# Optimization experiments

Hardware: AMD Instinct MI355X
Metric: run time of the kernel (lower is better)

Reference implementation:

```python
import jax, jax.numpy as jnp
import numpy as np

T, B, I, H = 1024, 64, 512, 512


def setup_inputs() -> dict:
    key = jax.random.key(0)
    ks = jax.random.split(key, 16)
    s = 0.05  # weight init scale
    inp = {
        "x": jax.random.normal(ks[0], (T, B, I), jnp.float32),
        "h0": jax.random.normal(ks[1], (B, H), jnp.float32),
        "c0": jax.random.normal(ks[2], (B, H), jnp.float32),
        "W_ih0f": jax.random.normal(ks[3], (4 * H, I), jnp.float32) * s,
        "W_hh0f": jax.random.normal(ks[4], (4 * H, H), jnp.float32) * s,
        "b0f": jax.random.normal(ks[5], (4 * H,), jnp.float32) * s,
        "W_ih0b": jax.random.normal(ks[6], (4 * H, I), jnp.float32) * s,
        "W_hh0b": jax.random.normal(ks[7], (4 * H, H), jnp.float32) * s,
        "b0b": jax.random.normal(ks[8], (4 * H,), jnp.float32) * s,
        "W_ih1f": jax.random.normal(ks[9], (4 * H, 2 * H), jnp.float32) * s,
        "W_hh1f": jax.random.normal(ks[10], (4 * H, H), jnp.float32) * s,
        "b1f": jax.random.normal(ks[11], (4 * H,), jnp.float32) * s,
        "W_ih1b": jax.random.normal(ks[12], (4 * H, 2 * H), jnp.float32) * s,
        "W_hh1b": jax.random.normal(ks[13], (4 * H, H), jnp.float32) * s,
        "b1b": jax.random.normal(ks[14], (4 * H,), jnp.float32) * s,
    }
    return inp


def _lstm_dir(x, h0, c0, W_ih, W_hh, b, reverse):
    # x: [T, B, in]; precompute input contribution once (big GEMM)
    xg = jnp.einsum('tbi,gi->tbg', x, W_ih) + b  # [T, B, 4H]

    def step(carry, xt):
        h, c = carry
        g = xt + h @ W_hh.T  # [B, 4H]
        i, f, gg, o = jnp.split(g, 4, axis=-1)  # PyTorch LSTMCell gate order
        i = jax.nn.sigmoid(i)
        f = jax.nn.sigmoid(f)
        gg = jnp.tanh(gg)
        o = jax.nn.sigmoid(o)
        c2 = f * c + i * gg
        h2 = o * jnp.tanh(c2)
        return (h2, c2), h2

    (hT, cT), out = jax.lax.scan(step, (h0, c0), xg, reverse=reverse)
    return out, hT, cT  # out[t] aligned with input time t


def reference(x, h0, c0,
              W_ih0f, W_hh0f, b0f, W_ih0b, W_hh0b, b0b,
              W_ih1f, W_hh1f, b1f, W_ih1b, W_hh1b, b1b):
    layers = [
        ((W_ih0f, W_hh0f, b0f), (W_ih0b, W_hh0b, b0b)),
        ((W_ih1f, W_hh1f, b1f), (W_ih1b, W_hh1b, b1b)),
    ]
    inputs = x
    hn, cn = [], []
    for (fw, bw) in layers:
        # NOTE: original reuses the same init_hidden for every layer/direction
        out_f, hf, cf = _lstm_dir(inputs, h0, c0, *fw, reverse=False)
        out_b, hb, cb = _lstm_dir(inputs, h0, c0, *bw, reverse=True)
        hn.append(jnp.concatenate([hf, hb], axis=1))
        cn.append(jnp.concatenate([cf, cb], axis=1))
        inputs = jnp.concatenate([out_f, out_b], axis=2)  # [T, B, 2H]
    hn = jnp.stack(hn, axis=0)  # [L, B, 2H]
    cn = jnp.stack(cn, axis=0)
    return inputs, hn, cn
```

## Files before the change

kernel.cpp:

```cpp
#include <hip/hip_runtime.h>


using bfrag = __attribute__((ext_vector_type(8))) short;
using facc  = __attribute__((ext_vector_type(4))) float;

#define TT 1024
#define NB 64

__device__ __forceinline__ unsigned short f2bf(float f) {
  union { float f; unsigned u; } v; v.f = f;
  unsigned r = v.u + 0x7fffu + ((v.u >> 16) & 1u);
  return (unsigned short)(r >> 16);
}
__device__ __forceinline__ float sigm(float x)  { return 1.f / (1.f + __expf(-x)); }
__device__ __forceinline__ float tanhf_(float x){ return 1.f - 2.f / (__expf(2.f * x) + 1.f); }

__device__ __forceinline__ facc mfma_bf16(bfrag a, bfrag b, facc c) {
  asm("v_mfma_f32_16x16x32_bf16 %0, %1, %2, %0" : "+v"(c) : "v"(a), "v"(b));
  return c;
}

__device__ __forceinline__ bfrag load_h16(const unsigned short* p) {
  union { unsigned long long q[2]; bfrag v; } u;
  const unsigned long long* qp = reinterpret_cast<const unsigned long long*>(p);
  u.q[0] = __hip_atomic_load(qp,     __ATOMIC_RELAXED, __HIP_MEMORY_SCOPE_AGENT);
  u.q[1] = __hip_atomic_load(qp + 1, __ATOMIC_RELAXED, __HIP_MEMORY_SCOPE_AGENT);
  return u.v;
}

__global__ __launch_bounds__(256) void k_cvt_x(const float* __restrict__ x,
                                               unsigned short* __restrict__ xb) {
  int i = blockIdx.x * 256 + threadIdx.x;
  float4 v = reinterpret_cast<const float4*>(x)[i];
  ushort4 o;
  o.x = f2bf(v.x); o.y = f2bf(v.y); o.z = f2bf(v.z); o.w = f2bf(v.w);
  reinterpret_cast<ushort4*>(xb)[i] = o;
}

__global__ __launch_bounds__(256) void k_init(const float* __restrict__ h0,
                                              unsigned short* __restrict__ h0b,
                                              unsigned* __restrict__ flags) {
  int i = blockIdx.x * 256 + threadIdx.x;
  h0b[i] = f2bf(h0[i]);
  if (i < 8192) flags[i] = 0;
}

template <int KX>
__global__ __launch_bounds__(256) void k_pack(const float* __restrict__ Wih,
                                              const float* __restrict__ Whh,
                                              const float* __restrict__ bias,
                                              unsigned short* __restrict__ PW,
                                              float* __restrict__ PB) {
  constexpr int K = KX + 512;
  int tid = blockIdx.x * 256 + threadIdx.x;
  int R = tid / K;
  int k = tid - R * K;
  int g = R >> 4, r = R & 15;
  int q = r >> 2, gate = r & 3;
  int srow = gate * 512 + (g * 4 + q);
  float v = (k < KX) ? Wih[srow * KX + k] : Whh[srow * 512 + (k - KX)];
  int gb = R >> 5, rr = R & 31, cc = k >> 3;
  PW[(size_t)gb * (K / 8) * 272 + cc * 272 + rr * 8 + (k & 7)] = f2bf(v);
  if (k == 0) PB[R] = bias[srow];
}

template <int LAYER>
__global__ __launch_bounds__(512, 2) void k_scan(
    const unsigned short* __restrict__ xin,
    unsigned short* __restrict__ y0,
    float* __restrict__ dout,
    const unsigned short* __restrict__ h0b,
    const float* __restrict__ c0,
    unsigned short* __restrict__ hb,
    const unsigned short* __restrict__ PWf, const unsigned short* __restrict__ PWb,
    const float* __restrict__ PBf, const float* __restrict__ PBb,
    unsigned* __restrict__ flagF, unsigned* __restrict__ flagB) {
  constexpr int KX = (LAYER == 0) ? 512 : 1024;
  constexpr int K  = KX + 512;
  constexpr int CH = K / 8;
  extern __shared__ unsigned short Wlds[];

  const int bid = blockIdx.x;
  const int dir = bid >> 6;
  const int gb  = bid & 63;
  const int tid = threadIdx.x;
  unsigned* flags = dir ? flagB : flagF;
  const unsigned short* pw = (dir ? PWb : PWf) + (size_t)gb * CH * 272;
  const float* pb          = dir ? PBb : PBf;

  for (int i = tid; i < CH * 34; i += 512)
    reinterpret_cast<bfrag*>(Wlds)[i] = reinterpret_cast<const bfrag*>(pw)[i];
  __syncthreads();

  const int w = tid >> 6, lane = tid & 63;
  const int lr = lane & 15, lq = lane >> 4;
  const int grT = w & 1, bT = w >> 1;
  const int b    = bT * 16 + lr;
  const int hcol = (gb * 2 + grT) * 4 + lq;
  const int ldsBase = grT * 128 + lr * 8;
  const float4 bias = *reinterpret_cast<const float4*>(pb + (gb * 2 + grT) * 16 + lq * 4);
  float c = c0[b * 512 + hcol];

  for (int s = 0; s < TT; ++s) {
    const int t = dir ? (TT - 1 - s) : s;

    const unsigned short* xrow = xin + ((size_t)t * NB + b) * KX + lq * 8;
    facc a0 = {0.f, 0.f, 0.f, 0.f}, a1 = {0.f, 0.f, 0.f, 0.f};
    asm volatile("s_nop 3" : "+v"(a0), "+v"(a1));
#pragma unroll 8
    for (int kk = 0; kk < KX / 32; ++kk) {
      bfrag a = *reinterpret_cast<const bfrag*>(Wlds + (size_t)(kk * 4 + lq) * 272 + ldsBase);
      bfrag x = *reinterpret_cast<const bfrag*>(xrow + kk * 32);
      if (kk & 1) a1 = mfma_bf16(a, x, a1); else a0 = mfma_bf16(a, x, a0);
    }

    if (s > 0) {
      if (w == 0) {
        unsigned* fl = flags + lane * 32;
        while (__hip_atomic_load(fl, __ATOMIC_RELAXED, __HIP_MEMORY_SCOPE_AGENT) < (unsigned)s)
          __builtin_amdgcn_s_sleep(1);
      }
      __syncthreads();
    }

    const int tp = dir ? (t + 1) : (t - 1);
    const unsigned short* hrow;
    if (s == 0)               hrow = h0b + (size_t)b * 512 + lq * 8;
    else if constexpr (LAYER == 0)
                              hrow = y0 + ((size_t)tp * NB + b) * 1024 + dir * 512 + lq * 8;
    else                      hrow = hb + (size_t)(((s & 1) ^ 1) * 2 + dir) * 32768 + (size_t)b * 512 + lq * 8;
#pragma unroll 8
    for (int kk = 0; kk < 16; ++kk) {
      bfrag a = *reinterpret_cast<const bfrag*>(Wlds + (size_t)(KX / 8 + kk * 4 + lq) * 272 + ldsBase);
      bfrag h = load_h16(hrow + kk * 32);
      if (kk & 1) a1 = mfma_bf16(a, h, a1); else a0 = mfma_bf16(a, h, a0);
    }
    asm volatile("s_nop 7\n\ts_nop 7" : "+v"(a0), "+v"(a1));

    float ig = sigm(a0[0] + a1[0] + bias.x);
    float fg = sigm(a0[1] + a1[1] + bias.y);
    float gv = tanhf_(a0[2] + a1[2] + bias.z);
    float og = sigm(a0[3] + a1[3] + bias.w);
    c = fg * c + ig * gv;
    const float h2 = og * tanhf_(c);

    const size_t orow = ((size_t)t * NB + b) * 1024 + dir * 512 + hcol;
    if constexpr (LAYER == 0) {
      __hip_atomic_store(&y0[orow], f2bf(h2), __ATOMIC_RELAXED, __HIP_MEMORY_SCOPE_AGENT);
    } else {
      dout[orow] = h2;
      __hip_atomic_store(&hb[(size_t)((s & 1) * 2 + dir) * 32768 + (size_t)b * 512 + hcol],
                         f2bf(h2), __ATOMIC_RELAXED, __HIP_MEMORY_SCOPE_AGENT);
    }
    if (s == TT - 1) {
      const size_t oh = ((size_t)LAYER * NB + b) * 1024 + dir * 512 + hcol;
      dout[67108864 + oh] = h2;
      dout[67239936 + oh] = c;
    }

    __syncthreads();
    if (tid == 0) {
      asm volatile("s_waitcnt vmcnt(0)" ::: "memory");
      __hip_atomic_store(flags + gb * 32, (unsigned)(s + 1),
                         __ATOMIC_RELAXED, __HIP_MEMORY_SCOPE_AGENT);
    }
  }
}

extern "C" void kernel_launch(void* const* d_in, const int* in_sizes, int n_in,
                              void* d_out, int out_size, void* d_ws, size_t ws_size,
                              hipStream_t stream) {
  (void)in_sizes; (void)n_in; (void)out_size; (void)ws_size;
  const float* x  = (const float*)d_in[0];
  const float* h0 = (const float*)d_in[1];
  const float* c0 = (const float*)d_in[2];
  const float* W[12];
  for (int i = 0; i < 12; ++i) W[i] = (const float*)d_in[3 + i];

  char* ws = (char*)d_ws;
  unsigned short* xb   = (unsigned short*)(ws + 0ull);
  unsigned short* y0   = (unsigned short*)(ws + 67108864ull);
  unsigned short* h0b  = (unsigned short*)(ws + 201326592ull);
  unsigned short* PW0F = (unsigned short*)(ws + 201392128ull);
  unsigned short* PW0B = (unsigned short*)(ws + 205848576ull);
  unsigned short* PW1F = (unsigned short*)(ws + 210305024ull);
  unsigned short* PW1B = (unsigned short*)(ws + 216989696ull);
  float*          PB   = (float*)(ws + 223674368ull);
  unsigned short* hb   = (unsigned short*)(ws + 223707136ull);
  unsigned*       flg  = (unsigned*)(ws + 223969280ull);
  float* dout = (float*)d_out;

  k_cvt_x<<<32768, 256, 0, stream>>>(x, xb);
  k_init<<<128, 256, 0, stream>>>(h0, h0b, flg);
  k_pack<512> <<<8192, 256, 0, stream>>>(W[0], W[1],  W[2],  PW0F, PB + 0);
  k_pack<512> <<<8192, 256, 0, stream>>>(W[3], W[4],  W[5],  PW0B, PB + 2048);
  k_pack<1024><<<12288, 256, 0, stream>>>(W[6], W[7],  W[8],  PW1F, PB + 4096);
  k_pack<1024><<<12288, 256, 0, stream>>>(W[9], W[10], W[11], PW1B, PB + 6144);

  const unsigned short* xin0 = xb;
  const unsigned short* xin1 = y0;
  unsigned short* y0m = y0;
  unsigned short* y0n = nullptr;
  const unsigned short* h0bc = h0b;
  unsigned* f00 = flg + 0;    unsigned* f01 = flg + 2048;
  unsigned* f10 = flg + 4096; unsigned* f11 = flg + 6144;
  const unsigned short *pw0f = PW0F, *pw0b = PW0B, *pw1f = PW1F, *pw1b = PW1B;
  const float *pb0f = PB + 0, *pb0b = PB + 2048, *pb1f = PB + 4096, *pb1b = PB + 6144;

  void* args0[] = {(void*)&xin0, (void*)&y0m, (void*)&dout, (void*)&h0bc, (void*)&c0,
                   (void*)&hb, (void*)&pw0f, (void*)&pw0b, (void*)&pb0f, (void*)&pb0b,
                   (void*)&f00, (void*)&f01};
  void* args1[] = {(void*)&xin1, (void*)&y0n, (void*)&dout, (void*)&h0bc, (void*)&c0,
                   (void*)&hb, (void*)&pw1f, (void*)&pw1b, (void*)&pb1f, (void*)&pb1b,
                   (void*)&f10, (void*)&f11};

  (void)hipFuncSetAttribute((const void*)(&k_scan<0>),
                            hipFuncAttributeMaxDynamicSharedMemorySize, 69632);
  (void)hipFuncSetAttribute((const void*)(&k_scan<1>),
                            hipFuncAttributeMaxDynamicSharedMemorySize, 104448);
  (void)hipLaunchCooperativeKernel((const void*)(&k_scan<0>), dim3(128), dim3(512),
                                   args0, 69632, stream);
  (void)hipLaunchCooperativeKernel((const void*)(&k_scan<1>), dim3(128), dim3(512),
                                   args1, 104448, stream);
}
```

Baseline: 27.21 ms.

## Repack LSTM weights lane-contiguous, prefetch recurrent weights, streamline inter-block flag sync

Weight packing is changed so each lane's MFMA fragment sits contiguously per k-chunk, which removes the padded stride and shrinks LDS use. The recurrent weight fragments are loaded from LDS into registers before the flag wait, so that LDS latency overlaps the spin. Flags are packed densely and every wave polls them directly, which removes the wave-0 poll plus block barrier. The flag is now published before the layer-1 output store, and the explicit vmcnt wait is dropped. In exchange, register pressure rises from holding 16 fragments, and the cross-block ordering of the h stores relative to the flag now relies on the relaxed atomics and the barrier alone.

```diff
diff --git a/kernel.cpp b/kernel.cpp
--- a/kernel.cpp
+++ b/kernel.cpp
@@ -42,7 +42,7 @@
                                               unsigned* __restrict__ flags) {
   int i = blockIdx.x * 256 + threadIdx.x;
   h0b[i] = f2bf(h0[i]);
-  if (i < 8192) flags[i] = 0;
+  if (i < 4096) flags[i] = 0;
 }
 
 template <int KX>
@@ -59,8 +59,9 @@
   int q = r >> 2, gate = r & 3;
   int srow = gate * 512 + (g * 4 + q);
   float v = (k < KX) ? Wih[srow * KX + k] : Whh[srow * 512 + (k - KX)];
-  int gb = R >> 5, rr = R & 31, cc = k >> 3;
-  PW[(size_t)gb * (K / 8) * 272 + cc * 272 + rr * 8 + (k & 7)] = f2bf(v);
+  int gb = R >> 5, rr = R & 31, grT = rr >> 4, lr = rr & 15;
+  int kk = k >> 5, lq = (k >> 3) & 3, e = k & 7;
+  PW[((size_t)gb * (K / 32) + kk) * 1024 + grT * 512 + lq * 128 + lr * 8 + e] = f2bf(v);
   if (k == 0) PB[R] = bias[srow];
 }
 
@@ -77,7 +78,7 @@
     unsigned* __restrict__ flagF, unsigned* __restrict__ flagB) {
   constexpr int KX = (LAYER == 0) ? 512 : 1024;
   constexpr int K  = KX + 512;
-  constexpr int CH = K / 8;
+  constexpr int NF = (K / 32) * 128;
   extern __shared__ unsigned short Wlds[];
 
   const int bid = blockIdx.x;
@@ -85,10 +86,10 @@
   const int gb  = bid & 63;
   const int tid = threadIdx.x;
   unsigned* flags = dir ? flagB : flagF;
-  const unsigned short* pw = (dir ? PWb : PWf) + (size_t)gb * CH * 272;
+  const unsigned short* pw = (dir ? PWb : PWf) + (size_t)gb * (K / 32) * 1024;
   const float* pb          = dir ? PBb : PBf;
 
-  for (int i = tid; i < CH * 34; i += 512)
+  for (int i = tid; i < NF; i += 512)
     reinterpret_cast<bfrag*>(Wlds)[i] = reinterpret_cast<const bfrag*>(pw)[i];
   __syncthreads();
 
@@ -97,7 +98,7 @@
   const int grT = w & 1, bT = w >> 1;
   const int b    = bT * 16 + lr;
   const int hcol = (gb * 2 + grT) * 4 + lq;
-  const int ldsBase = grT * 128 + lr * 8;
+  const int ldsLane = grT * 512 + lane * 8;
   const float4 bias = *reinterpret_cast<const float4*>(pb + (gb * 2 + grT) * 16 + lq * 4);
   float c = c0[b * 512 + hcol];
 
@@ -107,20 +108,22 @@
     const unsigned short* xrow = xin + ((size_t)t * NB + b) * KX + lq * 8;
     facc a0 = {0.f, 0.f, 0.f, 0.f}, a1 = {0.f, 0.f, 0.f, 0.f};
     asm volatile("s_nop 3" : "+v"(a0), "+v"(a1));
-#pragma unroll 8
+#pragma unroll
     for (int kk = 0; kk < KX / 32; ++kk) {
-      bfrag a = *reinterpret_cast<const bfrag*>(Wlds + (size_t)(kk * 4 + lq) * 272 + ldsBase);
+      bfrag a = *reinterpret_cast<const bfrag*>(Wlds + kk * 1024 + ldsLane);
       bfrag x = *reinterpret_cast<const bfrag*>(xrow + kk * 32);
       if (kk & 1) a1 = mfma_bf16(a, x, a1); else a0 = mfma_bf16(a, x, a0);
     }
 
+    bfrag ah[16];
+#pragma unroll
+    for (int kk = 0; kk < 16; ++kk)
+      ah[kk] = *reinterpret_cast<const bfrag*>(Wlds + (KX / 32 + kk) * 1024 + ldsLane);
+
     if (s > 0) {
-      if (w == 0) {
-        unsigned* fl = flags + lane * 32;
-        while (__hip_atomic_load(fl, __ATOMIC_RELAXED, __HIP_MEMORY_SCOPE_AGENT) < (unsigned)s)
-          __builtin_amdgcn_s_sleep(1);
-      }
-      __syncthreads();
+      while (__hip_atomic_load(&flags[lane], __ATOMIC_RELAXED, __HIP_MEMORY_SCOPE_AGENT)
+             < (unsigned)s)
+        __builtin_amdgcn_s_sleep(1);
     }
 
     const int tp = dir ? (t + 1) : (t - 1);
@@ -129,11 +132,10 @@
     else if constexpr (LAYER == 0)
                               hrow = y0 + ((size_t)tp * NB + b) * 1024 + dir * 512 + lq * 8;
     else                      hrow = hb + (size_t)(((s & 1) ^ 1) * 2 + dir) * 32768 + (size_t)b * 512 + lq * 8;
-#pragma unroll 8
+#pragma unroll
     for (int kk = 0; kk < 16; ++kk) {
-      bfrag a = *reinterpret_cast<const bfrag*>(Wlds + (size_t)(KX / 8 + kk * 4 + lq) * 272 + ldsBase);
       bfrag h = load_h16(hrow + kk * 32);
-      if (kk & 1) a1 = mfma_bf16(a, h, a1); else a0 = mfma_bf16(a, h, a0);
+      if (kk & 1) a1 = mfma_bf16(ah[kk], h, a1); else a0 = mfma_bf16(ah[kk], h, a0);
     }
     asm volatile("s_nop 7\n\ts_nop 7" : "+v"(a0), "+v"(a1));
 
@@ -148,21 +150,18 @@
     if constexpr (LAYER == 0) {
       __hip_atomic_store(&y0[orow], f2bf(h2), __ATOMIC_RELAXED, __HIP_MEMORY_SCOPE_AGENT);
     } else {
-      dout[orow] = h2;
       __hip_atomic_store(&hb[(size_t)((s & 1) * 2 + dir) * 32768 + (size_t)b * 512 + hcol],
                          f2bf(h2), __ATOMIC_RELAXED, __HIP_MEMORY_SCOPE_AGENT);
     }
+    __syncthreads();
+    if (tid == 0)
+      __hip_atomic_store(&flags[gb], (unsigned)(s + 1),
+                         __ATOMIC_RELAXED, __HIP_MEMORY_SCOPE_AGENT);
+    if constexpr (LAYER == 1) dout[orow] = h2;
     if (s == TT - 1) {
       const size_t oh = ((size_t)LAYER * NB + b) * 1024 + dir * 512 + hcol;
       dout[67108864 + oh] = h2;
       dout[67239936 + oh] = c;
-    }
-
-    __syncthreads();
-    if (tid == 0) {
-      asm volatile("s_waitcnt vmcnt(0)" ::: "memory");
-      __hip_atomic_store(flags + gb * 32, (unsigned)(s + 1),
-                         __ATOMIC_RELAXED, __HIP_MEMORY_SCOPE_AGENT);
     }
   }
 }
@@ -202,8 +201,8 @@
   unsigned short* y0m = y0;
   unsigned short* y0n = nullptr;
   const unsigned short* h0bc = h0b;
-  unsigned* f00 = flg + 0;    unsigned* f01 = flg + 2048;
-  unsigned* f10 = flg + 4096; unsigned* f11 = flg + 6144;
+  unsigned* f00 = flg + 0;    unsigned* f01 = flg + 1024;
+  unsigned* f10 = flg + 2048; unsigned* f11 = flg + 3072;
   const unsigned short *pw0f = PW0F, *pw0b = PW0B, *pw1f = PW1F, *pw1b = PW1B;
   const float *pb0f = PB + 0, *pb0b = PB + 2048, *pb1f = PB + 4096, *pb1b = PB + 6144;
 
@@ -215,11 +214,11 @@
                    (void*)&f10, (void*)&f11};
 
   (void)hipFuncSetAttribute((const void*)(&k_scan<0>),
-                            hipFuncAttributeMaxDynamicSharedMemorySize, 69632);
+                            hipFuncAttributeMaxDynamicSharedMemorySize, 65536);
   (void)hipFuncSetAttribute((const void*)(&k_scan<1>),
-                            hipFuncAttributeMaxDynamicSharedMemorySize, 104448);
+                            hipFuncAttributeMaxDynamicSharedMemorySize, 98304);
   (void)hipLaunchCooperativeKernel((const void*)(&k_scan<0>), dim3(128), dim3(512),
-                                   args0, 69632, stream);
+                                   args0, 65536, stream);
   (void)hipLaunchCooperativeKernel((const void*)(&k_scan<1>), dim3(128), dim3(512),
-                                   args1, 104448, stream);
-}
+                                   args1, 98304, stream);
+}
```

Measured after the change: 26.70 ms. Within noise of the previous version (-1.9%).
